# Kernel tuning notes

Measured on AMD Instinct MI355X. Metric: run time of the kernel, lower is better.

Reference implementation:

```python
import jax, jax.numpy as jnp
import numpy as np

V = 32000; D = 256; H = 8; L = 2; FF = 1024; S = 512; B = 32
M = 4096          # mem_max_entries
NC = 10           # num_classes
K = 4             # retrieve top-k
TH = 0.5          # write threshold
EPS = 1e-8


def setup_inputs() -> dict:
    key = jax.random.key(0)
    ks = jax.random.split(key, 24)
    s = 0.02
    def nrm(k, shape):
        return jax.random.normal(k, shape, jnp.float32) * s
    return {
        "input_ids": jax.random.randint(ks[0], (B, S), 0, V),
        "tok_emb": nrm(ks[1], (V, D)),
        "pos_emb": nrm(ks[2], (S, D)),
        # per-layer params stacked on leading dim L
        "Wqkv": nrm(ks[3], (L, 3 * D, D)), "bqkv": jnp.zeros((L, 3 * D)),
        "Wo": nrm(ks[4], (L, D, D)), "bo": jnp.zeros((L, D)),
        "ln1_g": jnp.ones((L, D)), "ln1_b": jnp.zeros((L, D)),
        "W1": nrm(ks[5], (L, FF, D)), "b1": jnp.zeros((L, FF)),
        "W2": nrm(ks[6], (L, D, FF)), "b2": jnp.zeros((L, D)),
        "ln2_g": jnp.ones((L, D)), "ln2_b": jnp.zeros((L, D)),
        # write gate MLP (d -> d -> 1, sigmoid)
        "Wg1": nrm(ks[7], (D, D)), "bg1": jnp.zeros((D,)),
        "Wg2": nrm(ks[8], (1, D)), "bg2": jnp.zeros((1,)),
        # classifier
        "Wc": nrm(ks[9], (NC, D)), "bc": jnp.zeros((NC,)),
    }


def _layer_norm(x, g, b):
    m = x.mean(-1, keepdims=True)
    v = ((x - m) ** 2).mean(-1, keepdims=True)
    return (x - m) / jnp.sqrt(v + 1e-5) * g + b


def _encoder_layer(x, Wqkv, bqkv, Wo, bo, g1, b1, W1, bf1, W2, bf2, g2, b2):
    # post-LN TransformerEncoderLayer, relu activation, batch_first
    Bx, Sx, Dx = x.shape
    dh = Dx // H
    qkv = x @ Wqkv.T + bqkv                     # [B,S,3D]
    q, k, v = jnp.split(qkv, 3, axis=-1)
    def heads(t):
        return t.reshape(Bx, Sx, H, dh).transpose(0, 2, 1, 3)  # [B,H,S,dh]
    q, k, v = heads(q), heads(k), heads(v)
    scores = jnp.einsum("bhqd,bhkd->bhqk", q, k) / jnp.sqrt(jnp.float32(dh))
    attn = jax.nn.softmax(scores, axis=-1)
    o = jnp.einsum("bhqk,bhkd->bhqd", attn, v)
    o = o.transpose(0, 2, 1, 3).reshape(Bx, Sx, Dx)
    o = o @ Wo.T + bo
    x = _layer_norm(x + o, g1, b1)
    ff = jax.nn.relu(x @ W1.T + bf1) @ W2.T + bf2
    return _layer_norm(x + ff, g2, b2)


def reference(input_ids, tok_emb, pos_emb, Wqkv, bqkv, Wo, bo, ln1_g, ln1_b,
              W1, b1, W2, b2, ln2_g, ln2_b, Wg1, bg1, Wg2, bg2, Wc, bc):
    Bx, Sx = input_ids.shape
    x = tok_emb[input_ids] + pos_emb[jnp.arange(Sx)][None, :, :]
    for l in range(L):
        x = _encoder_layer(x, Wqkv[l], bqkv[l], Wo[l], bo[l], ln1_g[l], ln1_b[l],
                           W1[l], b1[l], W2[l], b2[l], ln2_g[l], ln2_b[l])
    h = x                                        # [B,S,D]
    cls_state = h[:, 0, :]                       # [B,D]

    # --- write gate: per-token store into external memory (capped FIFO scatter) ---
    flat_h = h.reshape(-1, D)                    # [B*S, D]
    probs = jax.nn.sigmoid(jax.nn.relu(flat_h @ Wg1.T + bg1) @ Wg2.T + bg2)[:, 0]
    mask = probs > TH                            # [B*S]
    slot = jnp.cumsum(mask.astype(jnp.int32)) - 1
    valid = mask & (slot < M)
    idx = jnp.where(valid, slot, M)              # overflow -> dummy row M
    mem = jnp.zeros((M + 1, D), jnp.float32).at[idx].set(flat_h)[:M]
    count = jnp.minimum(mask.sum(), M)
    occupied = jnp.arange(M) < count             # [M]

    # --- top-k cosine retrieval with CLS as query ---
    qn = cls_state / (jnp.linalg.norm(cls_state, axis=-1, keepdims=True) + EPS)
    kn = mem / (jnp.linalg.norm(mem, axis=-1, keepdims=True) + EPS)
    sims = qn @ kn.T                             # [B,M]
    sims = jnp.where(occupied[None, :], sims, -1e9)
    top_sims, top_idx = jax.lax.top_k(sims, K)   # [B,K]
    vals = mem[top_idx]                          # [B,K,D] (unoccupied rows are zero)
    attn = jax.nn.softmax(top_sims, axis=-1)
    mem_vec = jnp.einsum("bk,bkd->bd", attn, vals)
    mem_vec = jnp.where(count > 0, mem_vec, 0.0)

    cls_aug = cls_state + mem_vec
    return cls_aug @ Wc.T + bc                   # [B,NC]
```

## Files before the change

### kernel.cpp

```cpp
#include <hip/hip_runtime.h>
#include <math.h>

#define D_   256
#define H_   8
#define L_   2
#define FF_  1024
#define S_   512
#define B_   32
#define M_   4096
#define NC_  10
#define ROWS (B_*S_)

typedef __attribute__((ext_vector_type(8))) short bf16x8;
typedef __attribute__((ext_vector_type(4))) float f32x4;
typedef unsigned int uint32;

__device__ __forceinline__ float wave_sum(float v) {
#pragma unroll
  for (int off = 1; off < 64; off <<= 1) v += __shfl_xor(v, off, 64);
  return v;
}

__device__ __forceinline__ unsigned short bf16_rne(float x) {
  unsigned int b = __float_as_uint(x);
  return (unsigned short)((b + 0x7FFFu + ((b >> 16) & 1u)) >> 16);
}
__device__ __forceinline__ float bf16_f(unsigned short h) {
  return __uint_as_float(((unsigned int)h) << 16);
}
__device__ __forceinline__ uint32 pack_split(float x) {
  const unsigned short h = bf16_rne(x);
  const unsigned short l = bf16_rne(x - bf16_f(h));
  return (uint32)h | ((uint32)l << 16);
}
__device__ __forceinline__ float unsplit(uint32 p) {
  return __uint_as_float(p << 16) + __uint_as_float(p & 0xffff0000u);
}
__device__ __forceinline__ void unpack_store(unsigned short* Hq, unsigned short* Lq,
                                             int off, uint4 v) {
  uint2 hp, lp;
  hp.x = (v.x & 0xffffu) | (v.y << 16);
  hp.y = (v.z & 0xffffu) | (v.w << 16);
  lp.x = (v.x >> 16) | (v.y & 0xffff0000u);
  lp.y = (v.z >> 16) | (v.w & 0xffff0000u);
  *(uint2*)&Hq[off] = hp;
  *(uint2*)&Lq[off] = lp;
}
__device__ __forceinline__ bf16x8 ld_frag(const unsigned short* p, int off) {
  union { uint2 u[2]; bf16x8 v; } x;
  x.u[0] = *(const uint2*)(p + off);
  x.u[1] = *(const uint2*)(p + off + 4);
  return x.v;
}

__global__ __launch_bounds__(256) void pack_f32(const float* __restrict__ src,
                                                uint32* __restrict__ dst, int n4) {
  const int i = blockIdx.x * 256 + threadIdx.x;
  if (i < n4) {
    const float4 v = ((const float4*)src)[i];
    uint4 o;
    o.x = pack_split(v.x); o.y = pack_split(v.y);
    o.z = pack_split(v.z); o.w = pack_split(v.w);
    ((uint4*)dst)[i] = o;
  }
}

__global__ __launch_bounds__(256) void emb_kernel(const int* __restrict__ ids,
                                                  const float* __restrict__ tok,
                                                  const float* __restrict__ pos,
                                                  uint32* __restrict__ xp) {
  const int row  = blockIdx.x * 4 + (threadIdx.x >> 6);
  const int lane = threadIdx.x & 63;
  const int id = ids[row];
  const int s  = row & (S_ - 1);
  const float4 t = *(const float4*)(tok + (size_t)id * D_ + lane * 4);
  const float4 p = *(const float4*)(pos + (size_t)s  * D_ + lane * 4);
  uint4 o;
  o.x = pack_split(t.x + p.x); o.y = pack_split(t.y + p.y);
  o.z = pack_split(t.z + p.z); o.w = pack_split(t.w + p.w);
  *(uint4*)(xp + (size_t)row * D_ + lane * 4) = o;
}

#define LP 36
template<int RELU>
__global__ __launch_bounds__(256, 2) void gemm_mfma(const uint32* __restrict__ Ap,
                                                    const uint32* __restrict__ Bp,
                                                    const float* __restrict__ bias,
                                                    uint32* __restrict__ Cp,
                                                    int K, int N, int NX) {
  __shared__ __align__(16) unsigned short Ah[128 * LP];
  __shared__ __align__(16) unsigned short Al[128 * LP];
  __shared__ __align__(16) unsigned short Bh[128 * LP];
  __shared__ __align__(16) unsigned short Bl[128 * LP];

  const int q8 = gridDim.x >> 3;
  const int orig = (blockIdx.x & 7) * q8 + (blockIdx.x >> 3);
  const int by = orig / NX, bx = orig % NX;
  const int m0 = by * 128, n0 = bx * 128;

  const int tid  = threadIdx.x;
  const int lane = tid & 63;
  const int wid  = tid >> 6;
  const int wm = wid >> 1, wn = wid & 1;
  const int lrow  = lane & 15;
  const int khalf = (lane >> 4) * 8;

  const int srow = tid >> 3;
  const int kq   = (tid & 7) << 2;
  const uint32* Aptr = Ap + (size_t)(m0 + srow) * K + kq;
  const uint32* Bptr = Bp + (size_t)(n0 + srow) * K + kq;

  f32x4 acc[4][4];
#pragma unroll
  for (int i = 0; i < 4; i++)
#pragma unroll
    for (int j = 0; j < 4; j++) acc[i][j] = (f32x4){0.f, 0.f, 0.f, 0.f};

  uint4 pa[4], pb[4];
#pragma unroll
  for (int j = 0; j < 4; j++) {
    pa[j] = *(const uint4*)(Aptr + (size_t)j * 32 * K);
    pb[j] = *(const uint4*)(Bptr + (size_t)j * 32 * K);
  }

  for (int k0 = 0; k0 < K; k0 += 32) {
    const int kn = (k0 + 32 < K) ? (k0 + 32) : k0;
    uint4 na[4], nb[4];
#pragma unroll
    for (int j = 0; j < 4; j++) {
      na[j] = *(const uint4*)(Aptr + (size_t)j * 32 * K + kn);
      nb[j] = *(const uint4*)(Bptr + (size_t)j * 32 * K + kn);
    }

    __syncthreads();
#pragma unroll
    for (int j = 0; j < 4; j++) {
      unpack_store(Ah, Al, (srow + j * 32) * LP + kq, pa[j]);
      unpack_store(Bh, Bl, (srow + j * 32) * LP + kq, pb[j]);
    }
    __syncthreads();

    bf16x8 ah[4], al[4], bh[4], bl[4];
#pragma unroll
    for (int f = 0; f < 4; f++) {
      const int rA = (wm * 64 + f * 16 + lrow) * LP + khalf;
      const int rB = (wn * 64 + f * 16 + lrow) * LP + khalf;
      ah[f] = ld_frag(Ah, rA);
      al[f] = ld_frag(Al, rA);
      bh[f] = ld_frag(Bh, rB);
      bl[f] = ld_frag(Bl, rB);
    }
#pragma unroll
    for (int fm = 0; fm < 4; fm++)
#pragma unroll
      for (int fn = 0; fn < 4; fn++) {
        acc[fm][fn] = __builtin_amdgcn_mfma_f32_16x16x32_bf16(ah[fm], bh[fn], acc[fm][fn], 0, 0, 0);
        acc[fm][fn] = __builtin_amdgcn_mfma_f32_16x16x32_bf16(ah[fm], bl[fn], acc[fm][fn], 0, 0, 0);
        acc[fm][fn] = __builtin_amdgcn_mfma_f32_16x16x32_bf16(al[fm], bh[fn], acc[fm][fn], 0, 0, 0);
      }
#pragma unroll
    for (int j = 0; j < 4; j++) { pa[j] = na[j]; pb[j] = nb[j]; }
  }

#pragma unroll
  for (int fm = 0; fm < 4; fm++)
#pragma unroll
    for (int fn = 0; fn < 4; fn++) {
      const int mrow = m0 + wm * 64 + fm * 16 + (lane >> 4) * 4;
      const int ncol = n0 + wn * 64 + fn * 16 + (lane & 15);
      const float bi = bias[ncol];
#pragma unroll
      for (int r = 0; r < 4; r++) {
        float v = acc[fm][fn][r] + bi;
        if (RELU) v = fmaxf(v, 0.f);
        Cp[(size_t)(mrow + r) * N + ncol] = pack_split(v);
      }
    }
}

template<int MODE>
__global__ __launch_bounds__(512, 2) void gemm_ln(const uint32* __restrict__ Ap,
                                                  const uint32* __restrict__ Bp,
                                                  const float* __restrict__ bias,
                                                  const uint32* __restrict__ residP,
                                                  const float* __restrict__ g,
                                                  const float* __restrict__ beta,
                                                  const float* __restrict__ Wg2,
                                                  const float* __restrict__ bg2,
                                                  uint32* __restrict__ outP,
                                                  int* __restrict__ mask,
                                                  int K) {
  __shared__ __align__(16) unsigned short Ah[64 * LP];
  __shared__ __align__(16) unsigned short Al[64 * LP];
  __shared__ __align__(16) unsigned short Bh[256 * LP];
  __shared__ __align__(16) unsigned short Bl[256 * LP];
  __shared__ float psumS[4][64];
  __shared__ float psumQ[4][64];
  __shared__ float meanL[64];
  __shared__ float invL[64];

  const int q8 = gridDim.x >> 3;
  const int m0 = ((blockIdx.x & 7) * q8 + (blockIdx.x >> 3)) * 64;

  const int tid  = threadIdx.x;
  const int lane = tid & 63;
  const int wid  = tid >> 6;
  const int wm = wid >> 2, wn = wid & 3;
  const int lrow  = lane & 15;
  const int khalf = (lane >> 4) * 8;

  const int srow = tid >> 3;
  const int kq   = (tid & 7) << 2;
  const uint32* Aptr = Ap + (size_t)(m0 + srow) * K + kq;
  const uint32* Bptr = Bp + (size_t)srow * K + kq;

  f32x4 acc[2][4];
#pragma unroll
  for (int i = 0; i < 2; i++)
#pragma unroll
    for (int j = 0; j < 4; j++) acc[i][j] = (f32x4){0.f, 0.f, 0.f, 0.f};

  uint4 pa, pb[4];
  pa = *(const uint4*)Aptr;
#pragma unroll
  for (int j = 0; j < 4; j++) pb[j] = *(const uint4*)(Bptr + (size_t)j * 64 * K);

  for (int k0 = 0; k0 < K; k0 += 32) {
    const int kn = (k0 + 32 < K) ? (k0 + 32) : k0;
    uint4 na, nb[4];
    na = *(const uint4*)(Aptr + kn);
#pragma unroll
    for (int j = 0; j < 4; j++) nb[j] = *(const uint4*)(Bptr + (size_t)j * 64 * K + kn);

    __syncthreads();
    unpack_store(Ah, Al, srow * LP + kq, pa);
#pragma unroll
    for (int j = 0; j < 4; j++)
      unpack_store(Bh, Bl, (srow + j * 64) * LP + kq, pb[j]);
    __syncthreads();

    bf16x8 ah[2], al[2], bh[4], bl[4];
#pragma unroll
    for (int fm = 0; fm < 2; fm++) {
      const int r = (wm * 32 + fm * 16 + lrow) * LP + khalf;
      ah[fm] = ld_frag(Ah, r);
      al[fm] = ld_frag(Al, r);
    }
#pragma unroll
    for (int fn = 0; fn < 4; fn++) {
      const int r = (wn * 64 + fn * 16 + lrow) * LP + khalf;
      bh[fn] = ld_frag(Bh, r);
      bl[fn] = ld_frag(Bl, r);
    }
#pragma unroll
    for (int fm = 0; fm < 2; fm++)
#pragma unroll
      for (int fn = 0; fn < 4; fn++) {
        acc[fm][fn] = __builtin_amdgcn_mfma_f32_16x16x32_bf16(ah[fm], bh[fn], acc[fm][fn], 0, 0, 0);
        acc[fm][fn] = __builtin_amdgcn_mfma_f32_16x16x32_bf16(ah[fm], bl[fn], acc[fm][fn], 0, 0, 0);
        acc[fm][fn] = __builtin_amdgcn_mfma_f32_16x16x32_bf16(al[fm], bh[fn], acc[fm][fn], 0, 0, 0);
      }
    pa = na;
#pragma unroll
    for (int j = 0; j < 4; j++) pb[j] = nb[j];
  }

  int cc[4];
  float bi[4];
#pragma unroll
  for (int fn = 0; fn < 4; fn++) {
    cc[fn] = wn * 64 + fn * 16 + (lane & 15);
    bi[fn] = bias[cc[fn]];
  }

  float vv[2][4][4];
  float rs[2][4], rq[2][4];

  if (MODE == 0) {
#pragma unroll
    for (int fm = 0; fm < 2; fm++)
#pragma unroll
      for (int r = 0; r < 4; r++) {
        const int row = m0 + wm * 32 + fm * 16 + (lane >> 4) * 4 + r;
        float s = 0.f, q = 0.f;
#pragma unroll
        for (int fn = 0; fn < 4; fn++) {
          const float rx = unsplit(residP[(size_t)row * 256 + cc[fn]]);
          const float a = acc[fm][fn][r] + bi[fn] + rx;
          vv[fm][fn][r] = a;
          s += a; q += a * a;
        }
        rs[fm][r] = s; rq[fm][r] = q;
      }
  } else {
    float wg[4];
#pragma unroll
    for (int fn = 0; fn < 4; fn++) wg[fn] = Wg2[cc[fn]];
#pragma unroll
    for (int fm = 0; fm < 2; fm++)
#pragma unroll
      for (int r = 0; r < 4; r++) {
        float s = 0.f;
#pragma unroll
        for (int fn = 0; fn < 4; fn++)
          s += fmaxf(acc[fm][fn][r] + bi[fn], 0.f) * wg[fn];
        rs[fm][r] = s;
      }
  }

#pragma unroll
  for (int off = 1; off < 16; off <<= 1) {
#pragma unroll
    for (int fm = 0; fm < 2; fm++)
#pragma unroll
      for (int r = 0; r < 4; r++) {
        rs[fm][r] += __shfl_xor(rs[fm][r], off, 64);
        if (MODE == 0) rq[fm][r] += __shfl_xor(rq[fm][r], off, 64);
      }
  }
  if ((lane & 15) == 0) {
#pragma unroll
    for (int fm = 0; fm < 2; fm++)
#pragma unroll
      for (int r = 0; r < 4; r++) {
        const int rloc = wm * 32 + fm * 16 + (lane >> 4) * 4 + r;
        psumS[wn][rloc] = rs[fm][r];
        if (MODE == 0) psumQ[wn][rloc] = rq[fm][r];
      }
  }
  __syncthreads();
  if (tid < 64) {
    float s = 0.f, q = 0.f;
#pragma unroll
    for (int w = 0; w < 4; w++) {
      s += psumS[w][tid];
      if (MODE == 0) q += psumQ[w][tid];
    }
    if (MODE == 0) {
      const float mean = s * (1.f / 256.f);
      const float var = q * (1.f / 256.f) - mean * mean;
      meanL[tid] = mean;
      invL[tid] = rsqrtf(var + 1e-5f);
    } else {
      mask[m0 + tid] = (s + bg2[0]) > 0.f ? 1 : 0;
    }
  }
  if (MODE == 0) {
    __syncthreads();
#pragma unroll
    for (int fm = 0; fm < 2; fm++)
#pragma unroll
      for (int r = 0; r < 4; r++) {
        const int rloc = wm * 32 + fm * 16 + (lane >> 4) * 4 + r;
        const int row = m0 + rloc;
        const float mu = meanL[rloc], iv = invL[rloc];
#pragma unroll
        for (int fn = 0; fn < 4; fn++) {
          const float y = (vv[fm][fn][r] - mu) * iv * g[cc[fn]] + beta[cc[fn]];
          outP[(size_t)row * 256 + cc[fn]] = pack_split(y);
        }
      }
  }
}

#define KP 36
#define VP 516
__global__ __launch_bounds__(1024, 4) void attn_mfma(const uint32* __restrict__ qkv,
                                                     uint32* __restrict__ o) {
  __shared__ __align__(16) unsigned short Kh[512 * KP];
  __shared__ __align__(16) unsigned short Kl[512 * KP];
  __shared__ __align__(16) unsigned short Vth[32 * VP];
  __shared__ __align__(16) unsigned short Vtl[32 * VP];

  const int q8g = gridDim.x >> 3;
  const int obh = (blockIdx.x & 7) * q8g + (blockIdx.x >> 3);
  const int b = obh >> 3, h = obh & 7;
  const int tid = threadIdx.x;
  const int lane = tid & 63;
  const int wv = tid >> 6;
  const uint32* base = qkv + (size_t)b * (S_ * 768) + h * 32;

  if (tid < 512) {
    const int slot = tid;
    const int s5 = slot & 31;
    const int orig = (slot & ~31) + 8 * ((s5 >> 2) & 3) + ((s5 >> 4) << 2) + (s5 & 3);
    const uint32* p = base + (size_t)orig * 768 + 256;
#pragma unroll
    for (int j = 0; j < 8; j++)
      unpack_store(Kh, Kl, slot * KP + j * 4, *(const uint4*)(p + j * 4));
  } else {
    const int u  = tid - 512;
    const int kp = u & 255;
    const int dg = (u >> 8) * 16;
    const uint32* p0 = base + (size_t)(2 * kp) * 768 + 512 + dg;
    const uint32* p1 = p0 + 768;
    union { uint4 u4[4]; uint32 w[16]; } a0, a1;
#pragma unroll
    for (int i = 0; i < 4; i++) {
      a0.u4[i] = *(const uint4*)(p0 + i * 4);
      a1.u4[i] = *(const uint4*)(p1 + i * 4);
    }
#pragma unroll
    for (int d = 0; d < 16; d++) {
      const uint32 w0 = a0.w[d], w1 = a1.w[d];
      *(uint32*)&Vth[(dg + d) * VP + 2 * kp] = (w0 & 0xffffu) | (w1 << 16);
      *(uint32*)&Vtl[(dg + d) * VP + 2 * kp] = (w0 >> 16) | (w1 & 0xffff0000u);
    }
  }

  const int q0 = wv * 32;
  bf16x8 qh[2], ql[2];
#pragma unroll
  for (int f = 0; f < 2; f++) {
    const uint32* qp = base + (size_t)(q0 + f * 16 + (lane & 15)) * 768 + ((lane >> 4) * 8);
    union { uint4 u4[2]; uint32 w[8]; } qu;
    qu.u4[0] = *(const uint4*)qp;
    qu.u4[1] = *(const uint4*)(qp + 4);
    bf16x8 vh, vl;
#pragma unroll
    for (int j = 0; j < 8; j++) {
      const float qf = unsplit(qu.w[j]);
      const float sv = qf * 0.17677669529663687f;
      const unsigned short hh = bf16_rne(sv);
      vh[j] = (short)hh;
      vl[j] = (short)bf16_rne(sv - bf16_f(hh));
    }
    qh[f] = vh; ql[f] = vl;
  }

  __syncthreads();

  auto qk_tile = [&](int kt, f32x4 (&s)[2][2]) {
    bf16x8 kah[2], kal[2];
#pragma unroll
    for (int u = 0; u < 2; u++) {
      const int off = (kt + u * 16 + (lane & 15)) * KP + ((lane >> 4) * 8);
      kah[u] = ld_frag(Kh, off);
      kal[u] = ld_frag(Kl, off);
    }
#pragma unroll
    for (int u = 0; u < 2; u++)
#pragma unroll
      for (int f = 0; f < 2; f++) {
        f32x4 a = (f32x4){0.f, 0.f, 0.f, 0.f};
        a = __builtin_amdgcn_mfma_f32_16x16x32_bf16(kal[u], qh[f], a, 0, 0, 0);
        a = __builtin_amdgcn_mfma_f32_16x16x32_bf16(kah[u], ql[f], a, 0, 0, 0);
        a = __builtin_amdgcn_mfma_f32_16x16x32_bf16(kah[u], qh[f], a, 0, 0, 0);
        s[u][f] = a;
      }
  };

  f32x4 oacc[2][2];
#pragma unroll
  for (int i = 0; i < 2; i++)
#pragma unroll
    for (int j = 0; j < 2; j++) oacc[i][j] = (f32x4){0.f, 0.f, 0.f, 0.f};
  float lacc[2] = {0.f, 0.f};

  f32x4 sA[2][2], sB[2][2];
  qk_tile(0, sA);

  for (int kt = 0; kt < S_; kt += 32) {
    if (kt + 32 < S_) qk_tile(kt + 32, sB);

    bf16x8 vah[2], val[2];
#pragma unroll
    for (int df = 0; df < 2; df++) {
      const int off = (df * 16 + (lane & 15)) * VP + kt + ((lane >> 4) * 8);
      vah[df] = ld_frag(Vth, off);
      val[df] = ld_frag(Vtl, off);
    }
#pragma unroll
    for (int f = 0; f < 2; f++) {
      union { uint32 w[4]; bf16x8 v; } ph, pl;
#pragma unroll
      for (int u = 0; u < 2; u++) {
        const float p0 = __expf(sA[u][f][0]);
        const float p1 = __expf(sA[u][f][1]);
        const float p2 = __expf(sA[u][f][2]);
        const float p3 = __expf(sA[u][f][3]);
        lacc[f] += (p0 + p1) + (p2 + p3);
        unsigned int h01, h23;
        asm volatile("v_cvt_pk_bf16_f32 %0, %1, %2" : "=v"(h01) : "v"(p0), "v"(p1));
        asm volatile("v_cvt_pk_bf16_f32 %0, %1, %2" : "=v"(h23) : "v"(p2), "v"(p3));
        const float r0 = p0 - __uint_as_float(h01 << 16);
        const float r1 = p1 - __uint_as_float(h01 & 0xffff0000u);
        const float r2 = p2 - __uint_as_float(h23 << 16);
        const float r3 = p3 - __uint_as_float(h23 & 0xffff0000u);
        unsigned int l01, l23;
        asm volatile("v_cvt_pk_bf16_f32 %0, %1, %2" : "=v"(l01) : "v"(r0), "v"(r1));
        asm volatile("v_cvt_pk_bf16_f32 %0, %1, %2" : "=v"(l23) : "v"(r2), "v"(r3));
        ph.w[u * 2 + 0] = h01;
        ph.w[u * 2 + 1] = h23;
        pl.w[u * 2 + 0] = l01;
        pl.w[u * 2 + 1] = l23;
      }
#pragma unroll
      for (int df = 0; df < 2; df++) {
        oacc[df][f] = __builtin_amdgcn_mfma_f32_16x16x32_bf16(val[df], ph.v, oacc[df][f], 0, 0, 0);
        oacc[df][f] = __builtin_amdgcn_mfma_f32_16x16x32_bf16(vah[df], pl.v, oacc[df][f], 0, 0, 0);
        oacc[df][f] = __builtin_amdgcn_mfma_f32_16x16x32_bf16(vah[df], ph.v, oacc[df][f], 0, 0, 0);
      }
    }
    if (kt + 32 < S_) {
#pragma unroll
      for (int u = 0; u < 2; u++)
#pragma unroll
        for (int f = 0; f < 2; f++) sA[u][f] = sB[u][f];
    }
  }

#pragma unroll
  for (int f = 0; f < 2; f++) {
    lacc[f] += __shfl_xor(lacc[f], 16, 64);
    lacc[f] += __shfl_xor(lacc[f], 32, 64);
  }
#pragma unroll
  for (int f = 0; f < 2; f++) {
    const float inv = 1.f / lacc[f];
    const int q = q0 + f * 16 + (lane & 15);
    uint32* op = o + (size_t)(b * S_ + q) * D_ + h * 32;
#pragma unroll
    for (int df = 0; df < 2; df++) {
      const int dbase = df * 16 + (lane >> 4) * 4;
#pragma unroll
      for (int r = 0; r < 4; r++)
        op[dbase + r] = pack_split(oacc[df][f][r] * inv);
    }
  }
}

__global__ __launch_bounds__(256) void scan_kernel(const int* __restrict__ mask,
                                                   int* __restrict__ slots,
                                                   int* __restrict__ countp) {
  __shared__ int wtot[4];
  const int tid = threadIdx.x;
  const int lane = tid & 63, wid = tid >> 6;
  const int base = tid * 64;
  int s = 0;
#pragma unroll 8
  for (int i = 0; i < 64; i++) s += mask[base + i];
  int inc = s;
#pragma unroll
  for (int off = 1; off < 64; off <<= 1) {
    const int t = __shfl_up(inc, off, 64);
    if (lane >= off) inc += t;
  }
  if (lane == 63) wtot[wid] = inc;
  __syncthreads();
  int woff = 0;
#pragma unroll
  for (int w = 0; w < 4; w++) woff += (w < wid) ? wtot[w] : 0;
  const int total = wtot[0] + wtot[1] + wtot[2] + wtot[3];
  if (tid == 0) countp[0] = total < M_ ? total : M_;
  int run = woff + inc - s;
  for (int i = 0; i < 64; i++) {
    const int r = base + i;
    const int mk = mask[r];
    slots[r] = (mk && run < M_) ? run : -1;
    run += mk;
  }
}

__global__ __launch_bounds__(256) void scatter_kernel(const uint32* __restrict__ h,
                                                      const int* __restrict__ slots,
                                                      float* __restrict__ mem) {
  const int row  = blockIdx.x * 4 + (threadIdx.x >> 6);
  const int lane = threadIdx.x & 63;
  const int sl = slots[row];
  if (sl >= 0) {
    const uint4 p = *(const uint4*)(h + (size_t)row * D_ + lane * 4);
    float4 r;
    r.x = unsplit(p.x); r.y = unsplit(p.y);
    r.z = unsplit(p.z); r.w = unsplit(p.w);
    *(float4*)(mem + (size_t)sl * D_ + lane * 4) = r;
  }
}

__global__ __launch_bounds__(256) void qnorm_kernel(const uint32* __restrict__ h,
                                                    float* __restrict__ qden) {
  const int b    = blockIdx.x * 4 + (threadIdx.x >> 6);
  const int lane = threadIdx.x & 63;
  const uint4 p = *(const uint4*)(h + (size_t)b * S_ * D_ + lane * 4);
  const float x0 = unsplit(p.x), x1 = unsplit(p.y);
  const float x2 = unsplit(p.z), x3 = unsplit(p.w);
  float sq = x0 * x0 + x1 * x1 + x2 * x2 + x3 * x3;
  sq = wave_sum(sq);
  if (lane == 0) qden[b] = sqrtf(sq) + 1e-8f;
}

__global__ __launch_bounds__(256) void sims_kernel(const uint32* __restrict__ h,
                                                   const float* __restrict__ mem,
                                                   const float* __restrict__ qden,
                                                   const int* __restrict__ countp,
                                                   float* __restrict__ sims) {
  __shared__ float cls[B_ * D_];
  __shared__ float qd[B_];
  const int tid = threadIdx.x;
  const int lane = tid & 63, wid = tid >> 6;
  for (int i = tid; i < B_ * D_ / 4; i += 256) {
    const int flat = i * 4;
    const int b = flat >> 8, d = flat & 255;
    const uint4 p = *(const uint4*)(h + (size_t)b * S_ * D_ + d);
    float4 r;
    r.x = unsplit(p.x); r.y = unsplit(p.y);
    r.z = unsplit(p.z); r.w = unsplit(p.w);
    *(float4*)&cls[flat] = r;
  }
  if (tid < B_) qd[tid] = qden[tid];
  __syncthreads();
  const int count = countp[0];
  const int r = blockIdx.x * 4 + wid;
  const float4 m4 = *(const float4*)(mem + (size_t)r * D_ + lane * 4);
  float sq = m4.x * m4.x + m4.y * m4.y + m4.z * m4.z + m4.w * m4.w;
  sq = wave_sum(sq);
  const float rn = sqrtf(sq) + 1e-8f;
  if (r < count) {
    for (int b = 0; b < B_; b++) {
      const float4 c4 = *(const float4*)&cls[b * D_ + lane * 4];
      float dt = m4.x * c4.x + m4.y * c4.y + m4.z * c4.z + m4.w * c4.w;
      dt = wave_sum(dt);
      if (lane == 0) sims[b * M_ + r] = dt / (qd[b] * rn);
    }
  } else if (lane == 0) {
    for (int b = 0; b < B_; b++) sims[b * M_ + r] = -1e9f;
  }
}

__global__ __launch_bounds__(256) void topk_mix(const uint32* __restrict__ h,
                                                const float* __restrict__ mem,
                                                const float* __restrict__ simsg,
                                                const int* __restrict__ countp,
                                                const float* __restrict__ Wc,
                                                const float* __restrict__ bc,
                                                float* __restrict__ out) {
  __shared__ float sims[M_];
  __shared__ float cls[D_];
  __shared__ float wv4[4];
  __shared__ int   wi4[4];
  __shared__ float aug[D_];
  __shared__ float tv[4];
  __shared__ int   tix[4];

  const int b = blockIdx.x, tid = threadIdx.x;
  const int lane = tid & 63, wid = tid >> 6;
  const int count = countp[0];

  for (int i = tid; i < M_; i += 256) sims[i] = simsg[b * M_ + i];
  cls[tid] = unsplit(h[(size_t)b * S_ * D_ + tid]);
  __syncthreads();

  for (int k = 0; k < 4; k++) {
    float bv = -INFINITY; int bi = 1 << 30;
#pragma unroll
    for (int rr = 0; rr < M_ / 256; rr++) {
      const int r = tid + rr * 256;
      const float v = sims[r];
      if (v > bv || (v == bv && r < bi)) { bv = v; bi = r; }
    }
#pragma unroll
    for (int off = 1; off < 64; off <<= 1) {
      const float ov = __shfl_xor(bv, off, 64);
      const int   oi = __shfl_xor(bi, off, 64);
      if (ov > bv || (ov == bv && oi < bi)) { bv = ov; bi = oi; }
    }
    if (lane == 0) { wv4[wid] = bv; wi4[wid] = bi; }
    __syncthreads();
    if (tid == 0) {
      float bb = wv4[0]; int bbi = wi4[0];
#pragma unroll
      for (int i = 1; i < 4; i++)
        if (wv4[i] > bb || (wv4[i] == bb && wi4[i] < bbi)) { bb = wv4[i]; bbi = wi4[i]; }
      tv[k] = bb; tix[k] = bbi; sims[bbi] = -INFINITY;
    }
    __syncthreads();
  }

  float w[4];
  {
    const float mx = tv[0];
    float ws = 0.f;
#pragma unroll
    for (int k = 0; k < 4; k++) { w[k] = expf(tv[k] - mx); ws += w[k]; }
    const float inv = 1.f / ws;
#pragma unroll
    for (int k = 0; k < 4; k++) w[k] *= inv;
  }

  {
    float mv = 0.f;
    if (count > 0) {
#pragma unroll
      for (int k = 0; k < 4; k++) mv = fmaf(w[k], mem[(size_t)tix[k] * D_ + tid], mv);
    }
    aug[tid] = cls[tid] + mv;
  }
  __syncthreads();

  const float4 a4 = *(const float4*)&aug[lane * 4];
  for (int c = wid; c < NC_; c += 4) {
    const float4 wc = *(const float4*)(Wc + (size_t)c * D_ + lane * 4);
    float dt = a4.x * wc.x + a4.y * wc.y + a4.z * wc.z + a4.w * wc.w;
    dt = wave_sum(dt);
    if (lane == 0) out[b * NC_ + c] = dt + bc[c];
  }
}

extern "C" void kernel_launch(void* const* d_in, const int* in_sizes, int n_in,
                              void* d_out, int out_size, void* d_ws, size_t ws_size,
                              hipStream_t stream) {
  const int*   ids  = (const int*)d_in[0];
  const float* tok  = (const float*)d_in[1];
  const float* pos  = (const float*)d_in[2];
  const float* Wqkv = (const float*)d_in[3];
  const float* bqkv = (const float*)d_in[4];
  const float* Wo   = (const float*)d_in[5];
  const float* bo   = (const float*)d_in[6];
  const float* ln1g = (const float*)d_in[7];
  const float* ln1b = (const float*)d_in[8];
  const float* W1   = (const float*)d_in[9];
  const float* b1   = (const float*)d_in[10];
  const float* W2   = (const float*)d_in[11];
  const float* b2   = (const float*)d_in[12];
  const float* ln2g = (const float*)d_in[13];
  const float* ln2b = (const float*)d_in[14];
  const float* Wg1  = (const float*)d_in[15];
  const float* bg1  = (const float*)d_in[16];
  const float* Wg2  = (const float*)d_in[17];
  const float* bg2  = (const float*)d_in[18];
  const float* Wc   = (const float*)d_in[19];
  const float* bc   = (const float*)d_in[20];
  float* out = (float*)d_out;

  uint32* xAp   = (uint32*)d_ws;
  uint32* xBp   = xAp + (size_t)ROWS * D_;
  uint32* obp   = xBp + (size_t)ROWS * D_;
  uint32* bigp  = obp + (size_t)ROWS * D_;
  uint32* Wqkvp = bigp + (size_t)ROWS * FF_;
  uint32* Wop   = Wqkvp + (size_t)L_ * 768 * 256;
  uint32* W1p   = Wop   + (size_t)L_ * 256 * 256;
  uint32* W2p   = W1p   + (size_t)L_ * 1024 * 256;
  uint32* Wg1p  = W2p   + (size_t)L_ * 256 * 1024;
  float*  mem   = (float*)(Wg1p + 256 * 256);
  float*  qden  = mem + (size_t)M_ * D_;
  float*  sims  = qden + 64;
  int*    mask  = (int*)(sims + (size_t)B_ * M_);
  int*    slots = mask + ROWS;
  int*    cnt   = slots + ROWS;

  pack_f32<<<(L_ * 768 * 256 / 4 + 255) / 256, 256, 0, stream>>>(Wqkv, Wqkvp, L_ * 768 * 256 / 4);
  pack_f32<<<(L_ * 256 * 256 / 4 + 255) / 256, 256, 0, stream>>>(Wo, Wop, L_ * 256 * 256 / 4);
  pack_f32<<<(L_ * 1024 * 256 / 4 + 255) / 256, 256, 0, stream>>>(W1, W1p, L_ * 1024 * 256 / 4);
  pack_f32<<<(L_ * 256 * 1024 / 4 + 255) / 256, 256, 0, stream>>>(W2, W2p, L_ * 256 * 1024 / 4);
  pack_f32<<<(256 * 256 / 4 + 255) / 256, 256, 0, stream>>>(Wg1, Wg1p, 256 * 256 / 4);

  emb_kernel<<<ROWS / 4, 256, 0, stream>>>(ids, tok, pos, xAp);

  for (int l = 0; l < L_; l++) {
    gemm_mfma<0><<<768, 256, 0, stream>>>(
        xAp, Wqkvp + (size_t)l * 768 * 256, bqkv + l * 768, bigp, 256, 768, 6);
    attn_mfma<<<B_ * H_, 1024, 0, stream>>>(bigp, obp);
    gemm_ln<0><<<ROWS / 64, 512, 0, stream>>>(
        obp, Wop + (size_t)l * 256 * 256, bo + l * 256, xAp,
        ln1g + l * 256, ln1b + l * 256, nullptr, nullptr, xBp, nullptr, 256);
    gemm_mfma<1><<<1024, 256, 0, stream>>>(
        xBp, W1p + (size_t)l * 1024 * 256, b1 + l * 1024, bigp, 256, 1024, 8);
    gemm_ln<0><<<ROWS / 64, 512, 0, stream>>>(
        bigp, W2p + (size_t)l * 256 * 1024, b2 + l * 256, xBp,
        ln2g + l * 256, ln2b + l * 256, nullptr, nullptr, xAp, nullptr, 1024);
  }

  gemm_ln<1><<<ROWS / 64, 512, 0, stream>>>(
      xAp, Wg1p, bg1, nullptr, nullptr, nullptr, Wg2, bg2, nullptr, mask, 256);
  scan_kernel<<<1, 256, 0, stream>>>(mask, slots, cnt);
  (void)hipMemsetAsync(mem, 0, (size_t)M_ * D_ * sizeof(float), stream);
  scatter_kernel<<<ROWS / 4, 256, 0, stream>>>(xAp, slots, mem);

  qnorm_kernel<<<B_ / 4, 256, 0, stream>>>(xAp, qden);
  sims_kernel<<<M_ / 4, 256, 0, stream>>>(xAp, mem, qden, cnt, sims);
  topk_mix<<<B_, 256, 0, stream>>>(xAp, mem, sims, cnt, Wc, bc, out);
}
```

Baseline: 408.7 us.

## Pre-pack weights into MFMA fragment layout and load B directly from global

Weights are now packed once into a per-fragment layout that matches the MFMA register operand, so the GEMM kernels load B fragments straight from global memory into registers instead of staging them through shared memory. This removes the B shared-memory stores and loads and shrinks LDS usage, which may allow higher occupancy. In exchange, each wave issues its own global loads for B every k-step with no prefetch one iteration ahead, relying on cache hits for reuse across blocks. It also increases the number of pack kernel launches.

```diff
diff --git a/kernel.cpp b/kernel.cpp
--- a/kernel.cpp
+++ b/kernel.cpp
@@ -46,6 +46,19 @@
   *(uint2*)&Hq[off] = hp;
   *(uint2*)&Lq[off] = lp;
 }
+__device__ __forceinline__ void unpack_frag(const uint4 u0, const uint4 u1,
+                                            bf16x8* hi, bf16x8* lo) {
+  union { uint32 w[4]; bf16x8 v; } H, L;
+  H.w[0] = (u0.x & 0xffffu) | (u0.y << 16);
+  H.w[1] = (u0.z & 0xffffu) | (u0.w << 16);
+  H.w[2] = (u1.x & 0xffffu) | (u1.y << 16);
+  H.w[3] = (u1.z & 0xffffu) | (u1.w << 16);
+  L.w[0] = (u0.x >> 16) | (u0.y & 0xffff0000u);
+  L.w[1] = (u0.z >> 16) | (u0.w & 0xffff0000u);
+  L.w[2] = (u1.x >> 16) | (u1.y & 0xffff0000u);
+  L.w[3] = (u1.z >> 16) | (u1.w & 0xffff0000u);
+  *hi = H.v; *lo = L.v;
+}
 __device__ __forceinline__ bf16x8 ld_frag(const unsigned short* p, int off) {
   union { uint2 u[2]; bf16x8 v; } x;
   x.u[0] = *(const uint2*)(p + off);
@@ -53,16 +66,25 @@
   return x.v;
 }
 
-__global__ __launch_bounds__(256) void pack_f32(const float* __restrict__ src,
-                                                uint32* __restrict__ dst, int n4) {
+__global__ __launch_bounds__(256) void pack_wfrag(const float* __restrict__ W,
+                                                  uint32* __restrict__ dst,
+                                                  int N, int K) {
   const int i = blockIdx.x * 256 + threadIdx.x;
-  if (i < n4) {
-    const float4 v = ((const float4*)src)[i];
-    uint4 o;
-    o.x = pack_split(v.x); o.y = pack_split(v.y);
-    o.z = pack_split(v.z); o.w = pack_split(v.w);
-    ((uint4*)dst)[i] = o;
-  }
+  const int total = (N >> 4) * (K >> 5) * 64;
+  if (i >= total) return;
+  const int lane = i & 63;
+  const int frag = i >> 6;
+  const int ktiles = K >> 5;
+  const int nf = frag / ktiles, kt = frag % ktiles;
+  const int n = nf * 16 + (lane & 15);
+  const int k0 = kt * 32 + (lane >> 4) * 8;
+  const float* src = W + (size_t)n * K + k0;
+  uint32 p[8];
+#pragma unroll
+  for (int j = 0; j < 8; j++) p[j] = pack_split(src[j]);
+  uint32* d = dst + (size_t)frag * 512 + lane * 4;
+  *(uint4*)d = make_uint4(p[0], p[1], p[2], p[3]);
+  *(uint4*)(d + 256) = make_uint4(p[4], p[5], p[6], p[7]);
 }
 
 __global__ __launch_bounds__(256) void emb_kernel(const int* __restrict__ ids,
@@ -84,14 +106,12 @@
 #define LP 36
 template<int RELU>
 __global__ __launch_bounds__(256, 2) void gemm_mfma(const uint32* __restrict__ Ap,
-                                                    const uint32* __restrict__ Bp,
+                                                    const uint32* __restrict__ Wf,
                                                     const float* __restrict__ bias,
                                                     uint32* __restrict__ Cp,
                                                     int K, int N, int NX) {
   __shared__ __align__(16) unsigned short Ah[128 * LP];
   __shared__ __align__(16) unsigned short Al[128 * LP];
-  __shared__ __align__(16) unsigned short Bh[128 * LP];
-  __shared__ __align__(16) unsigned short Bl[128 * LP];
 
   const int q8 = gridDim.x >> 3;
   const int orig = (blockIdx.x & 7) * q8 + (blockIdx.x >> 3);
@@ -108,7 +128,12 @@
   const int srow = tid >> 3;
   const int kq   = (tid & 7) << 2;
   const uint32* Aptr = Ap + (size_t)(m0 + srow) * K + kq;
-  const uint32* Bptr = Bp + (size_t)(n0 + srow) * K + kq;
+
+  const int ktiles = K >> 5;
+  size_t fbase[4];
+#pragma unroll
+  for (int f = 0; f < 4; f++)
+    fbase[f] = (size_t)(((n0 + wn * 64 + f * 16) >> 4) * ktiles) * 512 + lane * 4;
 
   f32x4 acc[4][4];
 #pragma unroll
@@ -116,39 +141,37 @@
 #pragma unroll
     for (int j = 0; j < 4; j++) acc[i][j] = (f32x4){0.f, 0.f, 0.f, 0.f};
 
-  uint4 pa[4], pb[4];
-#pragma unroll
-  for (int j = 0; j < 4; j++) {
-    pa[j] = *(const uint4*)(Aptr + (size_t)j * 32 * K);
-    pb[j] = *(const uint4*)(Bptr + (size_t)j * 32 * K);
-  }
+  uint4 pa[4];
+#pragma unroll
+  for (int j = 0; j < 4; j++) pa[j] = *(const uint4*)(Aptr + (size_t)j * 32 * K);
 
   for (int k0 = 0; k0 < K; k0 += 32) {
+    uint4 b0[4], b1[4];
+#pragma unroll
+    for (int f = 0; f < 4; f++) {
+      const uint32* fb = Wf + fbase[f] + (size_t)(k0 >> 5) * 512;
+      b0[f] = *(const uint4*)fb;
+      b1[f] = *(const uint4*)(fb + 256);
+    }
     const int kn = (k0 + 32 < K) ? (k0 + 32) : k0;
-    uint4 na[4], nb[4];
-#pragma unroll
-    for (int j = 0; j < 4; j++) {
+    uint4 na[4];
+#pragma unroll
+    for (int j = 0; j < 4; j++)
       na[j] = *(const uint4*)(Aptr + (size_t)j * 32 * K + kn);
-      nb[j] = *(const uint4*)(Bptr + (size_t)j * 32 * K + kn);
-    }
 
     __syncthreads();
 #pragma unroll
-    for (int j = 0; j < 4; j++) {
+    for (int j = 0; j < 4; j++)
       unpack_store(Ah, Al, (srow + j * 32) * LP + kq, pa[j]);
-      unpack_store(Bh, Bl, (srow + j * 32) * LP + kq, pb[j]);
-    }
     __syncthreads();
 
     bf16x8 ah[4], al[4], bh[4], bl[4];
 #pragma unroll
     for (int f = 0; f < 4; f++) {
       const int rA = (wm * 64 + f * 16 + lrow) * LP + khalf;
-      const int rB = (wn * 64 + f * 16 + lrow) * LP + khalf;
       ah[f] = ld_frag(Ah, rA);
       al[f] = ld_frag(Al, rA);
-      bh[f] = ld_frag(Bh, rB);
-      bl[f] = ld_frag(Bl, rB);
+      unpack_frag(b0[f], b1[f], &bh[f], &bl[f]);
     }
 #pragma unroll
     for (int fm = 0; fm < 4; fm++)
@@ -159,7 +182,7 @@
         acc[fm][fn] = __builtin_amdgcn_mfma_f32_16x16x32_bf16(al[fm], bh[fn], acc[fm][fn], 0, 0, 0);
       }
 #pragma unroll
-    for (int j = 0; j < 4; j++) { pa[j] = na[j]; pb[j] = nb[j]; }
+    for (int j = 0; j < 4; j++) pa[j] = na[j];
   }
 
 #pragma unroll
@@ -180,7 +203,7 @@
 
 template<int MODE>
 __global__ __launch_bounds__(512, 2) void gemm_ln(const uint32* __restrict__ Ap,
-                                                  const uint32* __restrict__ Bp,
+                                                  const uint32* __restrict__ Wf,
                                                   const float* __restrict__ bias,
                                                   const uint32* __restrict__ residP,
                                                   const float* __restrict__ g,
@@ -192,8 +215,6 @@
                                                   int K) {
   __shared__ __align__(16) unsigned short Ah[64 * LP];
   __shared__ __align__(16) unsigned short Al[64 * LP];
-  __shared__ __align__(16) unsigned short Bh[256 * LP];
-  __shared__ __align__(16) unsigned short Bl[256 * LP];
   __shared__ float psumS[4][64];
   __shared__ float psumQ[4][64];
   __shared__ float meanL[64];
@@ -212,7 +233,12 @@
   const int srow = tid >> 3;
   const int kq   = (tid & 7) << 2;
   const uint32* Aptr = Ap + (size_t)(m0 + srow) * K + kq;
-  const uint32* Bptr = Bp + (size_t)srow * K + kq;
+
+  const int ktiles = K >> 5;
+  size_t fbase[4];
+#pragma unroll
+  for (int f = 0; f < 4; f++)
+    fbase[f] = (size_t)(((wn * 64 + f * 16) >> 4) * ktiles) * 512 + lane * 4;
 
   f32x4 acc[2][4];
 #pragma unroll
@@ -220,23 +246,21 @@
 #pragma unroll
     for (int j = 0; j < 4; j++) acc[i][j] = (f32x4){0.f, 0.f, 0.f, 0.f};
 
-  uint4 pa, pb[4];
-  pa = *(const uint4*)Aptr;
-#pragma unroll
-  for (int j = 0; j < 4; j++) pb[j] = *(const uint4*)(Bptr + (size_t)j * 64 * K);
+  uint4 pa = *(const uint4*)Aptr;
 
   for (int k0 = 0; k0 < K; k0 += 32) {
+    uint4 b0[4], b1[4];
+#pragma unroll
+    for (int f = 0; f < 4; f++) {
+      const uint32* fb = Wf + fbase[f] + (size_t)(k0 >> 5) * 512;
+      b0[f] = *(const uint4*)fb;
+      b1[f] = *(const uint4*)(fb + 256);
+    }
     const int kn = (k0 + 32 < K) ? (k0 + 32) : k0;
-    uint4 na, nb[4];
-    na = *(const uint4*)(Aptr + kn);
-#pragma unroll
-    for (int j = 0; j < 4; j++) nb[j] = *(const uint4*)(Bptr + (size_t)j * 64 * K + kn);
+    uint4 na = *(const uint4*)(Aptr + kn);
 
     __syncthreads();
     unpack_store(Ah, Al, srow * LP + kq, pa);
-#pragma unroll
-    for (int j = 0; j < 4; j++)
-      unpack_store(Bh, Bl, (srow + j * 64) * LP + kq, pb[j]);
     __syncthreads();
 
     bf16x8 ah[2], al[2], bh[4], bl[4];
@@ -247,11 +271,8 @@
       al[fm] = ld_frag(Al, r);
     }
 #pragma unroll
-    for (int fn = 0; fn < 4; fn++) {
-      const int r = (wn * 64 + fn * 16 + lrow) * LP + khalf;
-      bh[fn] = ld_frag(Bh, r);
-      bl[fn] = ld_frag(Bl, r);
-    }
+    for (int fn = 0; fn < 4; fn++)
+      unpack_frag(b0[fn], b1[fn], &bh[fn], &bl[fn]);
 #pragma unroll
     for (int fm = 0; fm < 2; fm++)
 #pragma unroll
@@ -261,8 +282,6 @@
         acc[fm][fn] = __builtin_amdgcn_mfma_f32_16x16x32_bf16(al[fm], bh[fn], acc[fm][fn], 0, 0, 0);
       }
     pa = na;
-#pragma unroll
-    for (int j = 0; j < 4; j++) pb[j] = nb[j];
   }
 
   int cc[4];
@@ -748,11 +767,17 @@
   int*    slots = mask + ROWS;
   int*    cnt   = slots + ROWS;
 
-  pack_f32<<<(L_ * 768 * 256 / 4 + 255) / 256, 256, 0, stream>>>(Wqkv, Wqkvp, L_ * 768 * 256 / 4);
-  pack_f32<<<(L_ * 256 * 256 / 4 + 255) / 256, 256, 0, stream>>>(Wo, Wop, L_ * 256 * 256 / 4);
-  pack_f32<<<(L_ * 1024 * 256 / 4 + 255) / 256, 256, 0, stream>>>(W1, W1p, L_ * 1024 * 256 / 4);
-  pack_f32<<<(L_ * 256 * 1024 / 4 + 255) / 256, 256, 0, stream>>>(W2, W2p, L_ * 256 * 1024 / 4);
-  pack_f32<<<(256 * 256 / 4 + 255) / 256, 256, 0, stream>>>(Wg1, Wg1p, 256 * 256 / 4);
+  for (int l = 0; l < L_; l++) {
+    pack_wfrag<<<(768 * 256 / 4 + 255) / 256, 256, 0, stream>>>(
+        Wqkv + (size_t)l * 768 * 256, Wqkvp + (size_t)l * 768 * 256, 768, 256);
+    pack_wfrag<<<(256 * 256 / 4 + 255) / 256, 256, 0, stream>>>(
+        Wo + (size_t)l * 256 * 256, Wop + (size_t)l * 256 * 256, 256, 256);
+    pack_wfrag<<<(1024 * 256 / 4 + 255) / 256, 256, 0, stream>>>(
+        W1 + (size_t)l * 1024 * 256, W1p + (size_t)l * 1024 * 256, 1024, 256);
+    pack_wfrag<<<(256 * 1024 / 4 + 255) / 256, 256, 0, stream>>>(
+        W2 + (size_t)l * 256 * 1024, W2p + (size_t)l * 256 * 1024, 256, 1024);
+  }
+  pack_wfrag<<<(256 * 256 / 4 + 255) / 256, 256, 0, stream>>>(Wg1, Wg1p, 256, 256);
 
   emb_kernel<<<ROWS / 4, 256, 0, stream>>>(ids, tok, pos, xAp);
 
```

New measurement: 416.1 us. Within noise of the previous version (+1.8%).
